# Optimization experiments

Measured on AMD Instinct MI355X. Metric: run time of the kernel, lower is better.

## Reference

```python
import jax, jax.numpy as jnp
import numpy as np

B, C_IN, H, W = 2, 128, 96, 320
CQ = C_IN // 4   # q/k channels = 32
D = 32           # number of disparities


def _groupnorm1(x, w, b, eps=1e-5):
    # GroupNorm with 1 group == LayerNorm over (C,H,W) per sample, per-channel affine
    mu = x.mean(axis=(1, 2, 3), keepdims=True)
    var = x.var(axis=(1, 2, 3), keepdims=True)
    return (x - mu) / jnp.sqrt(var + eps) * w[None, :, None, None] + b[None, :, None, None]


def _warp_volume(x, disp, directs):
    # Faithful to affine_grid + grid_sample(bilinear, border, align_corners=True)
    # with a pure horizontal shift: pixel offset = disp * direct * (W-1).
    Bx, C, Hx, Wx = x.shape
    d = directs.reshape(Bx, 1, 1)                       # [B,1,1]
    j = jnp.arange(Wx, dtype=x.dtype)
    pos = j[None, None, :] + disp[None, :, None] * d * (Wx - 1)   # [B,D,W]
    pos = jnp.clip(pos, 0.0, Wx - 1)                    # border padding
    x0 = jnp.clip(jnp.floor(pos).astype(jnp.int32), 0, Wx - 1)
    x1 = jnp.minimum(x0 + 1, Wx - 1)
    t = pos - x0.astype(x.dtype)                        # [B,D,W]

    def per_b(xb, i0, i1, tb):
        g0 = xb[:, :, i0]                                # [C,H,D,W]
        g1 = xb[:, :, i1]
        return g0 * (1.0 - tb) + g1 * tb

    warped = jax.vmap(per_b)(x, x0, x1, t)               # [B,C,H,D,W]
    return jnp.moveaxis(warped, 3, 4)                    # [B,C,H,W,D]


def setup_inputs() -> dict:
    key = jax.random.key(0)
    ks = jax.random.split(key, 12)
    s = lambda i, shape: jax.random.normal(ks[i], shape, jnp.float32) * 0.05
    return {
        "t_feat": jax.random.normal(ks[0], (B, C_IN, H, W), jnp.float32),
        "s_feat": jax.random.normal(ks[1], (B, C_IN, H, W), jnp.float32),
        "directs": jnp.ones((B, 1, 1, 1), jnp.float32),
        "disp": jnp.arange(D, dtype=jnp.float32) * 0.01,   # norm_disp_range
        "q_w": s(2, (CQ, C_IN)), "q_b": jnp.zeros((CQ,), jnp.float32),
        "k_w": s(3, (CQ, C_IN)), "k_b": jnp.zeros((CQ,), jnp.float32),
        "cf_w": s(4, (1, 1, 3, 3, 3)), "cf_b": jnp.zeros((1,), jnp.float32),
        "nt_w": jnp.ones((C_IN,), jnp.float32), "nt_b": jnp.zeros((C_IN,), jnp.float32),
        "nc_w": jnp.ones((D,), jnp.float32), "nc_b": jnp.zeros((D,), jnp.float32),
        "ce_w": s(5, (C_IN, D)), "ce_b": jnp.zeros((C_IN,), jnp.float32),
        "fa_w": s(6, (1, 2 * C_IN)), "fa_b": jnp.zeros((1,), jnp.float32),
        "rc_w": s(7, (C_IN, C_IN, 3, 3)), "rc_b": jnp.zeros((C_IN,), jnp.float32),
        "se_w1": s(8, (C_IN // 16, C_IN)),
        "se_w2": s(9, (C_IN, C_IN // 16)),
    }


def reference(t_feat, s_feat, directs, disp, q_w, q_b, k_w, k_b, cf_w, cf_b,
              nt_w, nt_b, nc_w, nc_b, ce_w, ce_b, fa_w, fa_b, rc_w, rc_b,
              se_w1, se_w2):
    eps = 1e-12
    # 1x1 q/k projections
    q = jnp.einsum('oc,bchw->bohw', q_w, t_feat) + q_b[None, :, None, None]
    k = jnp.einsum('oc,bchw->bohw', k_w, s_feat) + k_b[None, :, None, None]

    # per-disparity warp -> [B,Cq,H,W,D]
    warped = _warp_volume(k, disp, directs)

    # DAV with patch_size=1: per-pixel cosine similarity over channels
    qn = q / jnp.maximum(jnp.linalg.norm(q, axis=1, keepdims=True), eps)
    kn = warped / jnp.maximum(jnp.linalg.norm(warped, axis=1, keepdims=True), eps)
    sim = jnp.einsum('bchw,bchwd->bdhw', qn, kn)          # [B,D,H,W]

    # 3x3x3 cost filter (Conv3d 1->1, padding 1)
    cost = jax.lax.conv_general_dilated(
        sim[:, None], cf_w, (1, 1, 1), [(1, 1)] * 3,
        dimension_numbers=('NCDHW', 'OIDHW', 'NCDHW'))[:, 0] + cf_b[0]
    norm_cost = jax.nn.softmax(cost, axis=1)              # softmax over D

    t_n = _groupnorm1(t_feat, nt_w, nt_b)
    c_n = _groupnorm1(norm_cost, nc_w, nc_b)
    cost_feat = jnp.einsum('od,bdhw->bohw', ce_w, c_n) + ce_b[None, :, None, None]

    fusion_in = jnp.concatenate([t_n, cost_feat], axis=1)
    alpha = jax.nn.sigmoid(jnp.einsum('oc,bchw->bohw', fa_w, fusion_in)
                           + fa_b[None, :, None, None])
    fused = alpha * t_n + (1.0 - alpha) * cost_feat       # same spatial size, no interp

    # redu: reflection-pad 3x3 conv -> SE -> ELU
    xp = jnp.pad(fused, ((0, 0), (0, 0), (1, 1), (1, 1)), mode='reflect')
    x = jax.lax.conv_general_dilated(
        xp, rc_w, (1, 1), 'VALID',
        dimension_numbers=('NCHW', 'OIHW', 'NCHW')) + rc_b[None, :, None, None]
    y = x.mean(axis=(2, 3))                               # [B,C]
    y = jax.nn.relu(y @ se_w1.T)
    y = jax.nn.sigmoid(y @ se_w2.T)
    x = jax.nn.elu(x * y[:, :, None, None])
    return (x, norm_cost)
```

## Files before the change

kernel.cpp:

```cpp
#include <hip/hip_runtime.h>
#include <stdint.h>

#define CC    128
#define CQn   32
#define DD    32
#define IMG_H 96
#define IMG_W 320
#define HW    30720
#define NPIX  61440

#define OFF_Q     0
#define OFF_K     3932160
#define OFF_SIM   7864320
#define OFF_NCP   15728640
#define OFF_FUSED 0
#define OFF_WC    19660800
#define OFF_WQK   19955712
#define OFF_AP    19972096
#define OFF_MISC  19988480
#define OFF_ST    20000768

typedef _Float16 half_t;
typedef _Float16 f16x2 __attribute__((ext_vector_type(2)));
typedef _Float16 f16x8 __attribute__((ext_vector_type(8)));
typedef float    f32x4 __attribute__((ext_vector_type(4)));

__device__ __forceinline__ float fdot2f(f16x2 a, f16x2 b, float c){
#if __has_builtin(__builtin_amdgcn_fdot2)
  return __builtin_amdgcn_fdot2(a, b, c, false);
#else
  return c + (float)a.x*(float)b.x + (float)a.y*(float)b.y;
#endif
}

__device__ __forceinline__ void gld16(const half_t* g, half_t* l){
#if __has_builtin(__builtin_amdgcn_global_load_lds)
  __builtin_amdgcn_global_load_lds(
      (const __attribute__((address_space(1))) unsigned int*)g,
      (__attribute__((address_space(3))) unsigned int*)l, 16, 0, 0);
#else
  *(uint4*)l = *(const uint4*)g;
#endif
}

__global__ __launch_bounds__(256) void k0_prep(
    const float* __restrict__ rc_w, const float* __restrict__ q_w, const float* __restrict__ k_w,
    const float* __restrict__ ce_w, const float* __restrict__ ce_b,
    const float* __restrict__ fa_w, const float* __restrict__ nt_w, const float* __restrict__ nt_b,
    half_t* __restrict__ wconv, half_t* __restrict__ wqk, float* __restrict__ gbuf){
  int blk = blockIdx.x, tid = threadIdx.x;
  if (blk < 576){
    int idx = blk * 256 + tid;
    int j = idx & 7;
    int o = (idx >> 3) & 127;
    int g = idx >> 10;
    int kq = g & 3, q4 = (g >> 2) & 3, pos = g >> 4;
    int c = q4*32 + kq*8 + j;
    wconv[idx] = (half_t)rc_w[(o*128 + c)*9 + pos];
  } else if (blk < 608){
    int idx = (blk - 576) * 256 + tid;
    wqk[idx] = (half_t)(idx < 4096 ? q_w[idx] : k_w[idx - 4096]);
  } else {
    int t = tid;
    if (t < 32){
      float a = 0.f;
      for (int o = 0; o < 128; o++) a += fa_w[128 + o] * ce_w[o * 32 + t];
      gbuf[t] = a;
    } else if (t == 32){
      float a = 0.f;
      for (int o = 0; o < 128; o++) a += fa_w[128 + o] * ce_b[o];
      gbuf[32] = a;
    } else if (t == 33){
      float a = 0.f;
      for (int c = 0; c < 128; c++) a += fa_w[c] * nt_w[c];
      gbuf[33] = a;
    } else if (t == 34){
      float a = 0.f;
      for (int c = 0; c < 128; c++) a += fa_w[c] * nt_b[c];
      gbuf[34] = a;
    }
  }
}

__global__ __launch_bounds__(256) void k1_qk(
    const float* __restrict__ t_feat, const float* __restrict__ s_feat,
    const half_t* __restrict__ wqk, const float* __restrict__ q_b, const float* __restrict__ k_b,
    half_t* __restrict__ qbuf, half_t* __restrict__ kbuf,
    double* __restrict__ tsum, double* __restrict__ tsq){
  __shared__ half_t feat[256 * 136];
  __shared__ half_t outs[256 * 40];
  __shared__ float red1[4], red2[4];
  __shared__ float qbl[32], kbl[32];
  int tid = threadIdx.x;
  int b = blockIdx.x / 120;
  int pix0 = (blockIdx.x % 120) * 256;
  int lane = tid & 63, wid = tid >> 6;
  int quad = lane >> 4, l15 = lane & 15;
  if (tid < 32){ qbl[tid] = q_b[tid]; kbl[tid] = k_b[tid]; }

  for (int phase = 0; phase < 2; phase++){
    const float* src = (phase == 0 ? t_feat : s_feat) + (size_t)b * CC * HW + pix0 + tid;
    float s1 = 0.f, s2 = 0.f;
    for (int c = 0; c < 128; c += 2){
      float v0 = src[c * HW], v1 = src[(c + 1) * HW];
      if (phase == 0){ s1 += v0 + v1; s2 += v0 * v0 + v1 * v1; }
      *(f16x2*)&feat[tid * 136 + c] = f16x2{(half_t)v0, (half_t)v1};
    }
    if (phase == 0){
      #pragma unroll
      for (int off = 32; off > 0; off >>= 1){ s1 += __shfl_down(s1, off, 64); s2 += __shfl_down(s2, off, 64); }
      if (lane == 0){ red1[wid] = s1; red2[wid] = s2; }
    }
    __syncthreads();
    if (phase == 0 && tid == 0){
      atomicAdd(&tsum[b], (double)red1[0] + red1[1] + red1[2] + red1[3]);
      atomicAdd(&tsq[b],  (double)red2[0] + red2[1] + red2[2] + red2[3]);
    }
    const half_t* W = wqk + phase * 4096;
    f32x4 acc[2][4];
    #pragma unroll
    for (int m = 0; m < 2; m++)
      #pragma unroll
      for (int nt = 0; nt < 4; nt++) acc[m][nt] = (f32x4){0.f,0.f,0.f,0.f};
    #pragma unroll
    for (int q4 = 0; q4 < 4; q4++){
      f16x8 a0 = *(const f16x8*)&W[(l15) * 128 + q4*32 + quad*8];
      f16x8 a1 = *(const f16x8*)&W[(16 + l15) * 128 + q4*32 + quad*8];
      #pragma unroll
      for (int nt = 0; nt < 4; nt++){
        f16x8 bf = *(const f16x8*)&feat[(wid*64 + nt*16 + l15) * 136 + q4*32 + quad*8];
        acc[0][nt] = __builtin_amdgcn_mfma_f32_16x16x32_f16(a0, bf, acc[0][nt], 0, 0, 0);
        acc[1][nt] = __builtin_amdgcn_mfma_f32_16x16x32_f16(a1, bf, acc[1][nt], 0, 0, 0);
      }
    }
    const float* bl = phase == 0 ? qbl : kbl;
    #pragma unroll
    for (int m = 0; m < 2; m++)
      #pragma unroll
      for (int nt = 0; nt < 4; nt++)
        #pragma unroll
        for (int r = 0; r < 4; r++){
          int o = m*16 + quad*4 + r;
          outs[(wid*64 + nt*16 + l15) * 40 + o] = (half_t)(acc[m][nt][r] + bl[o]);
        }
    __syncthreads();
    {
      half_t* dst = (phase == 0 ? qbuf : kbuf) + (size_t)(b * HW + pix0 + tid) * 32;
      uint4* d4 = (uint4*)dst;
      const uint4* s4 = (const uint4*)&outs[tid * 40];
      d4[0] = s4[0]; d4[1] = s4[1]; d4[2] = s4[2]; d4[3] = s4[3];
    }
    __syncthreads();
  }
}

__global__ __launch_bounds__(320) void k2_sim(
    const half_t* __restrict__ qbuf, const half_t* __restrict__ kbuf,
    const float* __restrict__ directs, const float* __restrict__ disp,
    float* __restrict__ sim){
  __shared__ uint4 klds4[320 * 5];
  __shared__ float displ[32];
  int tid = threadIdx.x;
  int b = blockIdx.y, h = blockIdx.x;
  for (int u = tid; u < 1280; u += 320){
    int x = u >> 2, j = u & 3;
    klds4[x * 5 + j] = ((const uint4*)(kbuf + (size_t)(b * HW + h * IMG_W + x) * 32))[j];
  }
  if (tid < 32) displ[tid] = disp[tid];
  __syncthreads();
  int w = tid;
  float direct = directs[b];
  union U16 { uint4 u4[4]; f16x2 h2[16]; };
  U16 qu;
  {
    const uint4* qp = (const uint4*)(qbuf + (size_t)(b * HW + h * IMG_W + w) * 32);
    qu.u4[0] = qp[0]; qu.u4[1] = qp[1]; qu.u4[2] = qp[2]; qu.u4[3] = qp[3];
  }
  float nq2 = 0.f;
  #pragma unroll
  for (int i = 0; i < 16; i++) nq2 = fdot2f(qu.h2[i], qu.h2[i], nq2);
  float inv_q = 1.0f / fmaxf(sqrtf(nq2), 1e-12f);
  float* simb = sim + (size_t)b * DD * HW + h * IMG_W + w;
  for (int d = 0; d < 32; d++){
    float pos = (float)w + displ[d] * direct * (float)(IMG_W - 1);
    pos = fminf(fmaxf(pos, 0.0f), (float)(IMG_W - 1));
    int x0 = (int)pos;
    int x1 = min(x0 + 1, IMG_W - 1);
    half_t tt = (half_t)(pos - (float)x0);
    f16x2 t2 = {tt, tt};
    U16 k0u, k1u;
    const uint4* r0 = &klds4[x0 * 5];
    const uint4* r1 = &klds4[x1 * 5];
    #pragma unroll
    for (int j = 0; j < 4; j++){ k0u.u4[j] = r0[j]; k1u.u4[j] = r1[j]; }
    float dot = 0.f, n2 = 0.f;
    #pragma unroll
    for (int i = 0; i < 16; i++){
      f16x2 wv = k0u.h2[i] + t2 * (k1u.h2[i] - k0u.h2[i]);
      dot = fdot2f(wv, qu.h2[i], dot);
      n2  = fdot2f(wv, wv, n2);
    }
    simb[d * HW] = dot * inv_q / fmaxf(sqrtf(n2), 1e-12f);
  }
}

__global__ __launch_bounds__(320) void k3_cost(
    const float* __restrict__ sim, const float* __restrict__ cf_w,
    float* __restrict__ norm_cost, half_t* __restrict__ ncp,
    double* __restrict__ csum, double* __restrict__ csq){
  __shared__ float w3[27];
  __shared__ float red1[5], red2[5];
  int tid = threadIdx.x;
  if (tid < 27) w3[tid] = cf_w[tid];
  __syncthreads();
  int b = blockIdx.y, h = blockIdx.x, w = tid;
  float cost[32];
  #pragma unroll
  for (int d = 0; d < 32; d++) cost[d] = 0.f;
  const float* sb = sim + (size_t)b * DD * HW;
  #pragma unroll
  for (int i = 0; i < 3; i++){
    int hh = h + i - 1;
    if (hh < 0 || hh >= IMG_H) continue;
    #pragma unroll
    for (int j = 0; j < 3; j++){
      int ww = w + j - 1;
      bool ok = (ww >= 0 && ww < IMG_W);
      const float* col = sb + hh * IMG_W + (ok ? ww : 0);
      float w0 = w3[0*9 + i*3 + j], w1 = w3[1*9 + i*3 + j], w2 = w3[2*9 + i*3 + j];
      #pragma unroll
      for (int e = 0; e < 32; e++){
        float v = ok ? col[e * HW] : 0.f;
        if (e < 31) cost[e+1] += w0 * v;
        cost[e] += w1 * v;
        if (e > 0)  cost[e-1] += w2 * v;
      }
    }
  }
  float mx = cost[0];
  #pragma unroll
  for (int d = 1; d < 32; d++) mx = fmaxf(mx, cost[d]);
  float s = 0.f;
  #pragma unroll
  for (int d = 0; d < 32; d++){ cost[d] = expf(cost[d] - mx); s += cost[d]; }
  float inv = 1.0f / s;
  float s1 = 0.f, s2 = 0.f;
  float* nb = norm_cost + (size_t)b * DD * HW + h * IMG_W + w;
  #pragma unroll
  for (int d = 0; d < 32; d++){
    float nc = cost[d] * inv;
    cost[d] = nc;
    nb[d * HW] = nc;
    s1 += nc; s2 += nc * nc;
  }
  {
    union { f16x2 h2[16]; uint4 u4[4]; } u;
    #pragma unroll
    for (int i = 0; i < 16; i++) u.h2[i] = f16x2{(half_t)cost[2*i], (half_t)cost[2*i+1]};
    uint4* dst = (uint4*)(ncp + (size_t)(b * HW + h * IMG_W + w) * 32);
    dst[0] = u.u4[0]; dst[1] = u.u4[1]; dst[2] = u.u4[2]; dst[3] = u.u4[3];
  }
  #pragma unroll
  for (int off = 32; off > 0; off >>= 1){ s1 += __shfl_down(s1, off, 64); s2 += __shfl_down(s2, off, 64); }
  int lane = tid & 63, wid = tid >> 6;
  if (lane == 0){ red1[wid] = s1; red2[wid] = s2; }
  __syncthreads();
  if (tid == 0){
    double a1 = 0, a2 = 0;
    for (int i = 0; i < 5; i++){ a1 += red1[i]; a2 += red2[i]; }
    atomicAdd(&csum[b], a1);
    atomicAdd(&csq[b], a2);
  }
}

__global__ __launch_bounds__(256) void k35_prep(
    const float* __restrict__ ce_w, const float* __restrict__ ce_b,
    const float* __restrict__ nt_w, const float* __restrict__ nt_b,
    const float* __restrict__ nc_w, const float* __restrict__ nc_b,
    const float* __restrict__ fa_w, const float* __restrict__ fa_b,
    const double* __restrict__ tsum, const double* __restrict__ tsq,
    const double* __restrict__ csum, const double* __restrict__ csq,
    const float* __restrict__ gbuf, half_t* __restrict__ ap, float* __restrict__ biasp,
    float* __restrict__ tnA, float* __restrict__ tnB, float* __restrict__ h1g,
    float* __restrict__ gp, float* __restrict__ zc){
  int t = threadIdx.x;
  int b = t >> 7, o = t & 127;
  float mu_t  = (float)(tsum[b] * (1.0 / (128.0 * HW)));
  float var_t = (float)(tsq[b]  * (1.0 / (128.0 * HW))) - mu_t * mu_t;
  float inv_t = 1.0f / sqrtf(var_t + 1e-5f);
  float mu_c  = (float)(csum[b] * (1.0 / (32.0 * HW)));
  float var_c = (float)(csq[b]  * (1.0 / (32.0 * HW))) - mu_c * mu_c;
  float inv_c = 1.0f / sqrtf(var_c + 1e-5f);
  float bias = ce_b[o];
  half_t* apo = ap + (size_t)(b * 128 + o) * 32;
  for (int d = 0; d < 32; d++){
    float wv = ce_w[o * 32 + d];
    bias += wv * (nc_b[d] - nc_w[d] * inv_c * mu_c);
    apo[d] = (half_t)(wv * nc_w[d] * inv_c);
  }
  biasp[b * 128 + o] = bias;
  tnA[b * 128 + o] = inv_t * nt_w[o];
  tnB[b * 128 + o] = nt_b[o] - mu_t * inv_t * nt_w[o];
  h1g[b * 128 + o] = fa_w[o] * nt_w[o] * inv_t;
  if (o < 32) gp[b * 32 + o] = gbuf[o] * nc_w[o] * inv_c;
  if (o == 0){
    float z = gbuf[32] + gbuf[34] - mu_t * inv_t * gbuf[33] + fa_b[0];
    for (int d = 0; d < 32; d++) z += gbuf[d] * (nc_b[d] - nc_w[d] * inv_c * mu_c);
    zc[b] = z;
  }
}

__global__ __launch_bounds__(256) void k4_fuse(
    const float* __restrict__ t_feat, const half_t* __restrict__ ncp,
    const half_t* __restrict__ ap, const float* __restrict__ biasp,
    const float* __restrict__ tnA, const float* __restrict__ tnB,
    const float* __restrict__ h1g, const float* __restrict__ gp,
    const float* __restrict__ zc, half_t* __restrict__ fused){
  __shared__ half_t cf[128 * 136];
  __shared__ float alphas[128];
  __shared__ float zred[256];
  __shared__ float biasl[128], tnAl[128], tnBl[128];
  int tid = threadIdx.x;
  int b = blockIdx.x / 240;
  int pix0 = (blockIdx.x % 240) * 128;
  int lane = tid & 63, wid = tid >> 6, quad = lane >> 4, l15 = lane & 15;
  if (tid < 128){
    biasl[tid] = biasp[b * 128 + tid];
    tnAl[tid] = tnA[b * 128 + tid];
    tnBl[tid] = tnB[b * 128 + tid];
  }
  {
    int px = tid & 127, hf = tid >> 7;
    const float* tf = t_feat + (size_t)b * CC * HW + pix0 + px;
    float z = 0.f;
    for (int c = hf * 64; c < hf * 64 + 64; c++) z += h1g[b * 128 + c] * tf[c * HW];
    if (hf == 0){
      const half_t* np = ncp + (size_t)(b * HW + pix0 + px) * 32;
      for (int d = 0; d < 32; d++) z += gp[b * 32 + d] * (float)np[d];
    }
    zred[tid] = z;
  }
  __syncthreads();
  if (tid < 128){
    float z = zred[tid] + zred[tid + 128] + zc[b];
    alphas[tid] = 1.0f / (1.0f + expf(-z));
  }
  f32x4 acc[8][2];
  #pragma unroll
  for (int mt = 0; mt < 8; mt++){ acc[mt][0] = (f32x4){0,0,0,0}; acc[mt][1] = (f32x4){0,0,0,0}; }
  f16x8 bfr[2];
  #pragma unroll
  for (int nt = 0; nt < 2; nt++)
    bfr[nt] = *(const f16x8*)&ncp[(size_t)(b * HW + pix0 + wid*32 + nt*16 + l15) * 32 + quad * 8];
  #pragma unroll
  for (int mt = 0; mt < 8; mt++){
    f16x8 a = *(const f16x8*)&ap[(size_t)(b * 128 + mt*16 + l15) * 32 + quad * 8];
    acc[mt][0] = __builtin_amdgcn_mfma_f32_16x16x32_f16(a, bfr[0], acc[mt][0], 0, 0, 0);
    acc[mt][1] = __builtin_amdgcn_mfma_f32_16x16x32_f16(a, bfr[1], acc[mt][1], 0, 0, 0);
  }
  #pragma unroll
  for (int mt = 0; mt < 8; mt++)
    #pragma unroll
    for (int nt = 0; nt < 2; nt++)
      #pragma unroll
      for (int r = 0; r < 4; r++){
        int o = mt*16 + quad*4 + r;
        cf[(wid*32 + nt*16 + l15) * 136 + o] = (half_t)(acc[mt][nt][r] + biasl[o]);
      }
  __syncthreads();
  {
    int px = (wid & 1) * 64 + lane;
    int ob = (wid >> 1) * 64;
    float al = alphas[px];
    const float* tf = t_feat + (size_t)b * CC * HW + pix0 + px;
    for (int oo = 0; oo < 64; oo++){
      int o = ob + oo;
      float tn = tf[o * HW] * tnAl[o] + tnBl[o];
      float c = (float)cf[px * 136 + o];
      cf[px * 136 + o] = (half_t)(al * (tn - c) + c);
    }
  }
  __syncthreads();
  {
    int px = tid >> 1, hf = tid & 1;
    const uint4* srow = (const uint4*)&cf[px * 136 + hf * 64];
    uint4* drow = (uint4*)(fused + (size_t)(b * HW + pix0 + px) * 128 + hf * 64);
    #pragma unroll
    for (int j = 0; j < 8; j++) drow[j] = srow[j];
  }
}

__global__ __launch_bounds__(256, 1) void k5_conv(
    const half_t* __restrict__ fused, const half_t* __restrict__ wconv,
    const float* __restrict__ rc_b, float* __restrict__ xout, float* __restrict__ ysum){
  __shared__ half_t patch[10 * 34 * 136];
  __shared__ half_t wlds[2][16384];
  __shared__ float rcb[128];
  int tid = threadIdx.x;
  int b = blockIdx.z;
  int h0 = blockIdx.y * 8;
  int w0 = blockIdx.x * 32;
  int lane = tid & 63, wid = tid >> 6, quad = lane >> 4, l15 = lane & 15;
  if (tid < 128) rcb[tid] = rc_b[tid];

  {
    const half_t* g = wconv;
    #pragma unroll
    for (int i = 0; i < 8; i++) gld16(g + (i*256 + tid)*8, &wlds[0][(i*256 + tid)*8]);
  }
  for (int idx = tid; idx < 340 * 16; idx += 256){
    int pp = idx >> 4, j = idx & 15;
    int r = pp / 34, col = pp - r * 34;
    int hs = h0 + r - 1;  hs = hs < 0 ? 1 : (hs >= IMG_H ? 2*IMG_H - 2 - hs : hs);
    int ws = w0 + col - 1; ws = ws < 0 ? 1 : (ws >= IMG_W ? 2*IMG_W - 2 - ws : ws);
    const uint4* s = (const uint4*)(fused + (size_t)(b * HW + hs * IMG_W + ws) * 128) + j;
    *((uint4*)&patch[(r * 34 + col) * 136] + j) = *s;
  }
  __syncthreads();

  f32x4 acc[8][4];
  #pragma unroll
  for (int mt = 0; mt < 8; mt++)
    #pragma unroll
    for (int nt = 0; nt < 4; nt++) acc[mt][nt] = (f32x4){0.f,0.f,0.f,0.f};

  #pragma unroll
  for (int kh = 0; kh < 3; kh++){
    #pragma unroll
    for (int kw2 = 0; kw2 < 3; kw2++){
      int pos = kh * 3 + kw2;
      if (pos < 8){
        const half_t* g = wconv + (pos + 1) * 16384;
        half_t* lb = &wlds[(pos + 1) & 1][0];
        #pragma unroll
        for (int i = 0; i < 8; i++) gld16(g + (i*256 + tid)*8, lb + (i*256 + tid)*8);
      }
      const half_t* wb = &wlds[pos & 1][0];
      #pragma unroll
      for (int q4 = 0; q4 < 4; q4++){
        f16x8 A[8];
        #pragma unroll
        for (int mt = 0; mt < 8; mt++)
          A[mt] = *(const f16x8*)&wb[((q4*4 + quad)*128 + mt*16 + l15)*8];
        #pragma unroll
        for (int nt = 0; nt < 4; nt++){
          int prow = wid*2 + (nt >> 1) + kh;
          int pcol = (nt & 1)*16 + l15 + kw2;
          f16x8 B = *(const f16x8*)&patch[(prow*34 + pcol)*136 + q4*32 + quad*8];
          #pragma unroll
          for (int mt = 0; mt < 8; mt++)
            acc[mt][nt] = __builtin_amdgcn_mfma_f32_16x16x32_f16(A[mt], B, acc[mt][nt], 0, 0, 0);
        }
      }
      __syncthreads();
    }
  }

  #pragma unroll
  for (int mt = 0; mt < 8; mt++){
    float ysl[4] = {0.f, 0.f, 0.f, 0.f};
    #pragma unroll
    for (int nt = 0; nt < 4; nt++){
      int hh = h0 + wid*2 + (nt >> 1);
      int ww = w0 + (nt & 1)*16 + l15;
      #pragma unroll
      for (int r = 0; r < 4; r++){
        int o = mt*16 + quad*4 + r;
        float v = acc[mt][nt][r] + rcb[o];
        xout[((size_t)(b * CC + o) * IMG_H + hh) * IMG_W + ww] = v;
        float rv = v;
        rv += __shfl_xor(rv, 1, 64);
        rv += __shfl_xor(rv, 2, 64);
        rv += __shfl_xor(rv, 4, 64);
        rv += __shfl_xor(rv, 8, 64);
        ysl[r] += rv;
      }
    }
    if (l15 == 0){
      #pragma unroll
      for (int r = 0; r < 4; r++) atomicAdd(&ysum[b * CC + mt*16 + quad*4 + r], ysl[r]);
    }
  }
}

__global__ __launch_bounds__(256) void k6_se(
    const float* __restrict__ ysum, const float* __restrict__ se_w1,
    const float* __restrict__ se_w2, float* __restrict__ sescale){
  __shared__ float ym[256];
  __shared__ float y1[16];
  int t = threadIdx.x;
  ym[t] = ysum[t] * (1.0f / (float)HW);
  __syncthreads();
  if (t < 16){
    int b = t >> 3, j = t & 7;
    float a = 0.f;
    for (int o = 0; o < 128; o++) a += ym[b * 128 + o] * se_w1[j * 128 + o];
    y1[t] = fmaxf(a, 0.f);
  }
  __syncthreads();
  int b = t >> 7, o = t & 127;
  float a = 0.f;
  #pragma unroll
  for (int j = 0; j < 8; j++) a += y1[b * 8 + j] * se_w2[o * 8 + j];
  sescale[t] = 1.0f / (1.0f + expf(-a));
}

__global__ __launch_bounds__(256) void k7_elu(float* __restrict__ x, const float* __restrict__ sescale){
  int i4 = blockIdx.x * 256 + threadIdx.x;
  float4* xp = (float4*)x;
  float4 v = xp[i4];
  float s = sescale[i4 / 7680];
  float a = v.x * s, bb = v.y * s, c = v.z * s, d = v.w * s;
  v.x = a  > 0.f ? a  : expm1f(a);
  v.y = bb > 0.f ? bb : expm1f(bb);
  v.z = c  > 0.f ? c  : expm1f(c);
  v.w = d  > 0.f ? d  : expm1f(d);
  xp[i4] = v;
}

extern "C" void kernel_launch(void* const* d_in, const int* in_sizes, int n_in,
                              void* d_out, int out_size, void* d_ws, size_t ws_size,
                              hipStream_t stream){
  const float* t_feat = (const float*)d_in[0];
  const float* s_feat = (const float*)d_in[1];
  const float* directs = (const float*)d_in[2];
  const float* disp   = (const float*)d_in[3];
  const float* q_w = (const float*)d_in[4];
  const float* q_b = (const float*)d_in[5];
  const float* k_w = (const float*)d_in[6];
  const float* k_b = (const float*)d_in[7];
  const float* cf_w = (const float*)d_in[8];
  const float* nt_w = (const float*)d_in[10];
  const float* nt_b = (const float*)d_in[11];
  const float* nc_w = (const float*)d_in[12];
  const float* nc_b = (const float*)d_in[13];
  const float* ce_w = (const float*)d_in[14];
  const float* ce_b = (const float*)d_in[15];
  const float* fa_w = (const float*)d_in[16];
  const float* fa_b = (const float*)d_in[17];
  const float* rc_w = (const float*)d_in[18];
  const float* rc_b = (const float*)d_in[19];
  const float* se_w1 = (const float*)d_in[20];
  const float* se_w2 = (const float*)d_in[21];

  char* ws = (char*)d_ws;
  half_t* qbuf  = (half_t*)(ws + OFF_Q);
  half_t* kbuf  = (half_t*)(ws + OFF_K);
  float*  sim   = (float*)(ws + OFF_SIM);
  half_t* ncp   = (half_t*)(ws + OFF_NCP);
  half_t* fused = (half_t*)(ws + OFF_FUSED);
  half_t* wconv = (half_t*)(ws + OFF_WC);
  half_t* wqk   = (half_t*)(ws + OFF_WQK);
  half_t* ap    = (half_t*)(ws + OFF_AP);
  float*  biasp = (float*)(ws + OFF_MISC);
  float*  tnA   = (float*)(ws + OFF_MISC + 1024);
  float*  tnB   = (float*)(ws + OFF_MISC + 2048);
  float*  h1g   = (float*)(ws + OFF_MISC + 3072);
  float*  gp    = (float*)(ws + OFF_MISC + 4096);
  float*  zc    = (float*)(ws + OFF_MISC + 4352);
  char* st = ws + OFF_ST;
  double* tsum = (double*)(st + 0);
  double* tsq  = (double*)(st + 16);
  double* csum = (double*)(st + 32);
  double* csq  = (double*)(st + 48);
  float* ysum  = (float*)(st + 64);
  float* sescale = (float*)(st + 1088);
  float* gbuf  = (float*)(st + 2112);

  float* xout = (float*)d_out;
  float* norm_cost = (float*)d_out + 7864320;

  hipMemsetAsync(st, 0, 1088, stream);
  k0_prep<<<610, 256, 0, stream>>>(rc_w, q_w, k_w, ce_w, ce_b, fa_w, nt_w, nt_b, wconv, wqk, gbuf);
  k1_qk<<<240, 256, 0, stream>>>(t_feat, s_feat, wqk, q_b, k_b, qbuf, kbuf, tsum, tsq);
  k2_sim<<<dim3(96, 2), 320, 0, stream>>>(qbuf, kbuf, directs, disp, sim);
  k3_cost<<<dim3(96, 2), 320, 0, stream>>>(sim, cf_w, norm_cost, ncp, csum, csq);
  k35_prep<<<1, 256, 0, stream>>>(ce_w, ce_b, nt_w, nt_b, nc_w, nc_b, fa_w, fa_b,
                                  tsum, tsq, csum, csq, gbuf, ap, biasp, tnA, tnB, h1g, gp, zc);
  k4_fuse<<<480, 256, 0, stream>>>(t_feat, ncp, ap, biasp, tnA, tnB, h1g, gp, zc, fused);
  k5_conv<<<dim3(10, 12, 2), 256, 0, stream>>>(fused, wconv, rc_b, xout, ysum);
  k6_se<<<1, 256, 0, stream>>>(ysum, se_w1, se_w2, sescale);
  k7_elu<<<7680, 256, 0, stream>>>(xout, sescale);
}
```

Before: 343.1 us.

## Shrink q/k and conv tiles, drop LDS weight staging for occupancy

The q/k projection kernel now handles 128 pixels per block with two threads per pixel splitting the channel load, and it reuses the feature buffer for output staging. This halves LDS use and doubles the grid. The 3x3 conv kernel now processes 4 rows per block instead of 8 and splits output channels across waves. It reads weight fragments straight from global/L2 instead of double-buffering them through LDS, and allows two blocks per CU. This trades weight reuse from LDS for more parallelism and lower register/LDS pressure, at the risk of extra global weight traffic and more patch halo reloads.

After: 305.5 us. 11.0% less time.

```diff
diff --git a/kernel.cpp b/kernel.cpp
--- a/kernel.cpp
+++ b/kernel.cpp
@@ -30,16 +30,6 @@
   return __builtin_amdgcn_fdot2(a, b, c, false);
 #else
   return c + (float)a.x*(float)b.x + (float)a.y*(float)b.y;
-#endif
-}
-
-__device__ __forceinline__ void gld16(const half_t* g, half_t* l){
-#if __has_builtin(__builtin_amdgcn_global_load_lds)
-  __builtin_amdgcn_global_load_lds(
-      (const __attribute__((address_space(1))) unsigned int*)g,
-      (__attribute__((address_space(3))) unsigned int*)l, 16, 0, 0);
-#else
-  *(uint4*)l = *(const uint4*)g;
 #endif
 }
 
@@ -87,24 +77,24 @@
     const half_t* __restrict__ wqk, const float* __restrict__ q_b, const float* __restrict__ k_b,
     half_t* __restrict__ qbuf, half_t* __restrict__ kbuf,
     double* __restrict__ tsum, double* __restrict__ tsq){
-  __shared__ half_t feat[256 * 136];
-  __shared__ half_t outs[256 * 40];
+  __shared__ half_t feat[128 * 136];
   __shared__ float red1[4], red2[4];
   __shared__ float qbl[32], kbl[32];
   int tid = threadIdx.x;
-  int b = blockIdx.x / 120;
-  int pix0 = (blockIdx.x % 120) * 256;
+  int b = blockIdx.x / 240;
+  int pix0 = (blockIdx.x % 240) * 128;
   int lane = tid & 63, wid = tid >> 6;
   int quad = lane >> 4, l15 = lane & 15;
   if (tid < 32){ qbl[tid] = q_b[tid]; kbl[tid] = k_b[tid]; }
+  int px_s = tid & 127, hf = tid >> 7;
 
   for (int phase = 0; phase < 2; phase++){
-    const float* src = (phase == 0 ? t_feat : s_feat) + (size_t)b * CC * HW + pix0 + tid;
+    const float* src = (phase == 0 ? t_feat : s_feat) + (size_t)b * CC * HW + pix0 + px_s;
     float s1 = 0.f, s2 = 0.f;
-    for (int c = 0; c < 128; c += 2){
+    for (int c = hf * 64; c < hf * 64 + 64; c += 2){
       float v0 = src[c * HW], v1 = src[(c + 1) * HW];
       if (phase == 0){ s1 += v0 + v1; s2 += v0 * v0 + v1 * v1; }
-      *(f16x2*)&feat[tid * 136 + c] = f16x2{(half_t)v0, (half_t)v1};
+      *(f16x2*)&feat[px_s * 136 + c] = f16x2{(half_t)v0, (half_t)v1};
     }
     if (phase == 0){
       #pragma unroll
@@ -117,18 +107,16 @@
       atomicAdd(&tsq[b],  (double)red2[0] + red2[1] + red2[2] + red2[3]);
     }
     const half_t* W = wqk + phase * 4096;
-    f32x4 acc[2][4];
-    #pragma unroll
-    for (int m = 0; m < 2; m++)
-      #pragma unroll
-      for (int nt = 0; nt < 4; nt++) acc[m][nt] = (f32x4){0.f,0.f,0.f,0.f};
+    f32x4 acc[2][2];
+    #pragma unroll
+    for (int m = 0; m < 2; m++){ acc[m][0] = (f32x4){0,0,0,0}; acc[m][1] = (f32x4){0,0,0,0}; }
     #pragma unroll
     for (int q4 = 0; q4 < 4; q4++){
       f16x8 a0 = *(const f16x8*)&W[(l15) * 128 + q4*32 + quad*8];
       f16x8 a1 = *(const f16x8*)&W[(16 + l15) * 128 + q4*32 + quad*8];
       #pragma unroll
-      for (int nt = 0; nt < 4; nt++){
-        f16x8 bf = *(const f16x8*)&feat[(wid*64 + nt*16 + l15) * 136 + q4*32 + quad*8];
+      for (int nt = 0; nt < 2; nt++){
+        f16x8 bf = *(const f16x8*)&feat[(wid*32 + nt*16 + l15) * 136 + q4*32 + quad*8];
         acc[0][nt] = __builtin_amdgcn_mfma_f32_16x16x32_f16(a0, bf, acc[0][nt], 0, 0, 0);
         acc[1][nt] = __builtin_amdgcn_mfma_f32_16x16x32_f16(a1, bf, acc[1][nt], 0, 0, 0);
       }
@@ -137,18 +125,20 @@
     #pragma unroll
     for (int m = 0; m < 2; m++)
       #pragma unroll
-      for (int nt = 0; nt < 4; nt++)
+      for (int nt = 0; nt < 2; nt++)
         #pragma unroll
         for (int r = 0; r < 4; r++){
           int o = m*16 + quad*4 + r;
-          outs[(wid*64 + nt*16 + l15) * 40 + o] = (half_t)(acc[m][nt][r] + bl[o]);
+          feat[(wid*32 + nt*16 + l15) * 136 + o] = (half_t)(acc[m][nt][r] + bl[o]);
         }
     __syncthreads();
     {
-      half_t* dst = (phase == 0 ? qbuf : kbuf) + (size_t)(b * HW + pix0 + tid) * 32;
-      uint4* d4 = (uint4*)dst;
-      const uint4* s4 = (const uint4*)&outs[tid * 40];
-      d4[0] = s4[0]; d4[1] = s4[1]; d4[2] = s4[2]; d4[3] = s4[3];
+      half_t* dst = (phase == 0 ? qbuf : kbuf) + (size_t)(b * HW + pix0 + px_s) * 32;
+      if (hf == 0){
+        uint4* d4 = (uint4*)dst;
+        const uint4* s4 = (const uint4*)&feat[px_s * 136];
+        d4[0] = s4[0]; d4[1] = s4[1]; d4[2] = s4[2]; d4[3] = s4[3];
+      }
     }
     __syncthreads();
   }
@@ -390,25 +380,19 @@
   }
 }
 
-__global__ __launch_bounds__(256, 1) void k5_conv(
+__global__ __launch_bounds__(256, 2) void k5_conv(
     const half_t* __restrict__ fused, const half_t* __restrict__ wconv,
     const float* __restrict__ rc_b, float* __restrict__ xout, float* __restrict__ ysum){
-  __shared__ half_t patch[10 * 34 * 136];
-  __shared__ half_t wlds[2][16384];
+  __shared__ half_t patch[6 * 34 * 136];
   __shared__ float rcb[128];
   int tid = threadIdx.x;
   int b = blockIdx.z;
-  int h0 = blockIdx.y * 8;
+  int h0 = blockIdx.y * 4;
   int w0 = blockIdx.x * 32;
   int lane = tid & 63, wid = tid >> 6, quad = lane >> 4, l15 = lane & 15;
   if (tid < 128) rcb[tid] = rc_b[tid];
 
-  {
-    const half_t* g = wconv;
-    #pragma unroll
-    for (int i = 0; i < 8; i++) gld16(g + (i*256 + tid)*8, &wlds[0][(i*256 + tid)*8]);
-  }
-  for (int idx = tid; idx < 340 * 16; idx += 256){
+  for (int idx = tid; idx < 204 * 16; idx += 256){
     int pp = idx >> 4, j = idx & 15;
     int r = pp / 34, col = pp - r * 34;
     int hs = h0 + r - 1;  hs = hs < 0 ? 1 : (hs >= IMG_H ? 2*IMG_H - 2 - hs : hs);
@@ -418,54 +402,40 @@
   }
   __syncthreads();
 
-  f32x4 acc[8][4];
-  #pragma unroll
-  for (int mt = 0; mt < 8; mt++)
-    #pragma unroll
-    for (int nt = 0; nt < 4; nt++) acc[mt][nt] = (f32x4){0.f,0.f,0.f,0.f};
-
-  #pragma unroll
-  for (int kh = 0; kh < 3; kh++){
-    #pragma unroll
-    for (int kw2 = 0; kw2 < 3; kw2++){
-      int pos = kh * 3 + kw2;
-      if (pos < 8){
-        const half_t* g = wconv + (pos + 1) * 16384;
-        half_t* lb = &wlds[(pos + 1) & 1][0];
-        #pragma unroll
-        for (int i = 0; i < 8; i++) gld16(g + (i*256 + tid)*8, lb + (i*256 + tid)*8);
+  f32x4 acc[2][8];
+  #pragma unroll
+  for (int mt = 0; mt < 2; mt++)
+    #pragma unroll
+    for (int nt = 0; nt < 8; nt++) acc[mt][nt] = (f32x4){0.f,0.f,0.f,0.f};
+
+  for (int pos = 0; pos < 9; pos++){
+    int kh = pos / 3;
+    int kw2 = pos - kh * 3;
+    #pragma unroll
+    for (int q4 = 0; q4 < 4; q4++){
+      const half_t* wrow = wconv + ((size_t)(pos*16 + q4*4 + quad) * 128 + wid*32 + l15) * 8;
+      f16x8 A0 = *(const f16x8*)wrow;
+      f16x8 A1 = *(const f16x8*)(wrow + 128);
+      #pragma unroll
+      for (int nt = 0; nt < 8; nt++){
+        int hrow = nt >> 1, whalf = nt & 1;
+        f16x8 B = *(const f16x8*)&patch[((hrow + kh)*34 + whalf*16 + l15 + kw2)*136 + q4*32 + quad*8];
+        acc[0][nt] = __builtin_amdgcn_mfma_f32_16x16x32_f16(A0, B, acc[0][nt], 0, 0, 0);
+        acc[1][nt] = __builtin_amdgcn_mfma_f32_16x16x32_f16(A1, B, acc[1][nt], 0, 0, 0);
       }
-      const half_t* wb = &wlds[pos & 1][0];
-      #pragma unroll
-      for (int q4 = 0; q4 < 4; q4++){
-        f16x8 A[8];
-        #pragma unroll
-        for (int mt = 0; mt < 8; mt++)
-          A[mt] = *(const f16x8*)&wb[((q4*4 + quad)*128 + mt*16 + l15)*8];
-        #pragma unroll
-        for (int nt = 0; nt < 4; nt++){
-          int prow = wid*2 + (nt >> 1) + kh;
-          int pcol = (nt & 1)*16 + l15 + kw2;
-          f16x8 B = *(const f16x8*)&patch[(prow*34 + pcol)*136 + q4*32 + quad*8];
-          #pragma unroll
-          for (int mt = 0; mt < 8; mt++)
-            acc[mt][nt] = __builtin_amdgcn_mfma_f32_16x16x32_f16(A[mt], B, acc[mt][nt], 0, 0, 0);
-        }
-      }
-      __syncthreads();
-    }
-  }
-
-  #pragma unroll
-  for (int mt = 0; mt < 8; mt++){
+    }
+  }
+
+  #pragma unroll
+  for (int mt = 0; mt < 2; mt++){
     float ysl[4] = {0.f, 0.f, 0.f, 0.f};
     #pragma unroll
-    for (int nt = 0; nt < 4; nt++){
-      int hh = h0 + wid*2 + (nt >> 1);
+    for (int nt = 0; nt < 8; nt++){
+      int hh = h0 + (nt >> 1);
       int ww = w0 + (nt & 1)*16 + l15;
       #pragma unroll
       for (int r = 0; r < 4; r++){
-        int o = mt*16 + quad*4 + r;
+        int o = wid*32 + mt*16 + quad*4 + r;
         float v = acc[mt][nt][r] + rcb[o];
         xout[((size_t)(b * CC + o) * IMG_H + hh) * IMG_W + ww] = v;
         float rv = v;
@@ -478,7 +448,7 @@
     }
     if (l15 == 0){
       #pragma unroll
-      for (int r = 0; r < 4; r++) atomicAdd(&ysum[b * CC + mt*16 + quad*4 + r], ysl[r]);
+      for (int r = 0; r < 4; r++) atomicAdd(&ysum[b * CC + wid*32 + mt*16 + quad*4 + r], ysl[r]);
     }
   }
 }
@@ -572,13 +542,13 @@
 
   hipMemsetAsync(st, 0, 1088, stream);
   k0_prep<<<610, 256, 0, stream>>>(rc_w, q_w, k_w, ce_w, ce_b, fa_w, nt_w, nt_b, wconv, wqk, gbuf);
-  k1_qk<<<240, 256, 0, stream>>>(t_feat, s_feat, wqk, q_b, k_b, qbuf, kbuf, tsum, tsq);
+  k1_qk<<<480, 256, 0, stream>>>(t_feat, s_feat, wqk, q_b, k_b, qbuf, kbuf, tsum, tsq);
   k2_sim<<<dim3(96, 2), 320, 0, stream>>>(qbuf, kbuf, directs, disp, sim);
   k3_cost<<<dim3(96, 2), 320, 0, stream>>>(sim, cf_w, norm_cost, ncp, csum, csq);
   k35_prep<<<1, 256, 0, stream>>>(ce_w, ce_b, nt_w, nt_b, nc_w, nc_b, fa_w, fa_b,
                                   tsum, tsq, csum, csq, gbuf, ap, biasp, tnA, tnB, h1g, gp, zc);
   k4_fuse<<<480, 256, 0, stream>>>(t_feat, ncp, ap, biasp, tnA, tnB, h1g, gp, zc, fused);
-  k5_conv<<<dim3(10, 12, 2), 256, 0, stream>>>(fused, wconv, rc_b, xout, ysum);
+  k5_conv<<<dim3(10, 24, 2), 256, 0, stream>>>(fused, wconv, rc_b, xout, ysum);
   k6_se<<<1, 256, 0, stream>>>(ysum, se_w1, se_w2, sescale);
   k7_elu<<<7680, 256, 0, stream>>>(xout, sescale);
 }
```
